# Performance work log

Hardware: AMD Instinct MI355X
Metric: run time of the kernel (lower is better)

Reference implementation:

```python
import jax, jax.numpy as jnp
import numpy as np

WS = 7            # window size (fixed by RelativeEmbedding default)
EMBED = 96
HEADS = 3
BATCH = 64
SIDE = 56         # height = width = sqrt(3136)
NEG_INF = float('-inf')


def _rel_bias_from_table(b_np):
    # Faithful reproduction of RelativeEmbedding.__init__ indexing quirks:
    # x = arange(1, ws+1, 1/ws) -> 49 floats; diffs truncated toward zero (.int())
    x = np.arange(1, WS + 1, 1.0 / WS, dtype=np.float32)
    xi = np.trunc(x[None, :] - x[:, None]).astype(np.int64)  # in [-6, 6]
    y = np.concatenate([np.arange(1, WS + 1)] * WS)
    yi = (y[None, :] - y[:, None]).astype(np.int64)          # in [-6, 6]
    n = 2 * WS - 1  # 13; emulate torch negative indexing with mod
    return b_np[xi % n, yi % n]  # (49, 49)


def _shift_masks():
    m = WS * (WS // 2)  # 21
    row_mask = np.zeros((WS * WS, WS * WS), dtype=np.float32)
    row_mask[-m:, :-m] = NEG_INF
    row_mask[:-m, -m:] = NEG_INF
    # rearrange '(r w1) (c w2) -> (w1 r) (w2 c)'
    col_mask = row_mask.reshape(WS, WS, WS, WS).transpose(1, 0, 3, 2).reshape(WS * WS, WS * WS)
    return jnp.asarray(row_mask), jnp.asarray(col_mask)


def setup_inputs() -> dict:
    key = jax.random.key(0)
    k1, k2, k3, k4, k5, k6 = jax.random.split(key, 6)
    x = jax.random.normal(k1, (BATCH, SIDE * SIDE, EMBED), dtype=jnp.float32)
    w1 = jax.random.normal(k2, (EMBED, 3 * EMBED), dtype=jnp.float32) * 0.02
    b1 = jnp.zeros((3 * EMBED,), dtype=jnp.float32)
    w2 = jax.random.normal(k3, (EMBED, EMBED), dtype=jnp.float32) * 0.02
    b2 = jnp.zeros((EMBED,), dtype=jnp.float32)
    b_table = np.asarray(jax.random.normal(k4, (2 * WS - 1, 2 * WS - 1), dtype=jnp.float32))
    rel_bias = jnp.asarray(_rel_bias_from_table(b_table))  # (49, 49), non-trainable
    return {"x": x, "w1": w1, "b1": b1, "w2": w2, "b2": b2, "rel_bias": rel_bias}


def reference(x, w1, b1, w2, b2, rel_bias):
    Bz, N, C = x.shape
    side = SIDE
    H = HEADS
    E = C // H          # head dim = 32
    nh = side // WS     # 8 windows per side

    qkv = x @ w1 + b1                                   # (B, N, 3C)
    # 'b (h w) (c K) -> b h w c K' with K=3 fastest-varying
    qkv = qkv.reshape(Bz, side, side, C, 3)
    # shifted-window roll; note (-7)//2 == -4 in Python (faithful to source)
    qkv = jnp.roll(qkv, ((-WS) // 2, (-WS) // 2), axis=(1, 2))
    # 'b (h m1) (w m2) (H E) K -> b H h w (m1 m2) E K'
    qkv = qkv.reshape(Bz, nh, WS, nh, WS, H, E, 3)
    qkv = qkv.transpose(0, 5, 1, 3, 2, 4, 6, 7).reshape(Bz, H, nh, nh, WS * WS, E, 3)
    q, k, v = qkv[..., 0], qkv[..., 1], qkv[..., 2]

    scale = jnp.sqrt(jnp.float32(E))
    att = jnp.einsum('bHhwme,bHhwne->bHhwmn', q, k) / scale  # (B,H,8,8,49,49)
    att = att + rel_bias

    row_mask, col_mask = _shift_masks()
    att = att.at[:, :, -1, :].add(row_mask)   # last window row
    att = att.at[:, :, :, -1].add(col_mask)   # last window column

    p = jax.nn.softmax(att, axis=-1)
    out = jnp.einsum('bHhwmn,bHhwne->bHhwme', p, v)          # (B,H,8,8,49,32)

    # 'b H h w (m1 m2) E -> b (h m1) (w m2) (H E)'
    out = out.reshape(Bz, H, nh, nh, WS, WS, E)
    out = out.transpose(0, 2, 4, 3, 5, 1, 6).reshape(Bz, side, side, C)
    # reverse roll uses +(7//2) == +3 (faithful asymmetry in the source)
    out = jnp.roll(out, (WS // 2, WS // 2), axis=(1, 2))
    out = out.reshape(Bz, N, C)
    return out @ w2 + b2
```

## Files before the change

### kernel.cpp

```cpp
#include <hip/hip_runtime.h>
#include <hip/hip_fp16.h>

typedef _Float16 half8_t __attribute__((ext_vector_type(8)));
typedef _Float16 half4_t __attribute__((ext_vector_type(4)));
typedef float f32x4 __attribute__((ext_vector_type(4)));
typedef unsigned int u32x4 __attribute__((ext_vector_type(4)));

#define WS_W2T 55296
#define WS_B1P 73728
#define WS_TBL 74880

__global__ __launch_bounds__(256) void swin_prep_kernel(
    const float* __restrict__ w1, const float* __restrict__ b1,
    const float* __restrict__ w2, const float* __restrict__ relb,
    _Float16* __restrict__ w1T, _Float16* __restrict__ w2T,
    float* __restrict__ b1p, float* __restrict__ tblP)
{
    int idx = blockIdx.x * 256 + threadIdx.x;
    const float L2E = 1.4426950408889634f;
    const float qs2 = 0.17677669529663687f * L2E;
    if (idx < 27648) {
        int jp = idx / 96, k = idx % 96;
        float v;
        if (jp < 96) {
            int f = jp >> 4, m = jp & 15;
            int cq = (f >> 1) * 32 + (m >> 2) * 8 + (f & 1) * 4 + (m & 3);
            v = w1[k * 288 + cq * 3] * qs2;
        } else {
            int jo = (jp % 96) * 3 + (jp / 96);
            v = w1[k * 288 + jo];
        }
        w1T[idx] = (_Float16)v;
    } else if (idx < 36864) {
        int i2 = idx - 27648;
        int n = i2 / 96, k = i2 % 96;
        w2T[i2] = (_Float16)w2[k * 96 + n];
    } else if (idx < 37152) {
        int jp = idx - 36864;
        float v = b1[(jp % 96) * 3 + (jp / 96)];
        if (jp < 96) v *= qs2;
        b1p[jp] = v;
    } else if (idx < 53536) {
        int t = idx - 37152;
        int vv = t >> 12, q = (t >> 6) & 63, c = t & 63;
        int i = c >> 4, m = c & 15;
        int k = (i >> 1) * 32 + (m >> 2) * 8 + (i & 1) * 4 + (m & 3);
        float val = -1e30f;
        if (q < 49 && k < 49) {
            val = relb[q * 49 + k] * L2E;
            if ((vv & 1) && ((q >= 28) != (k >= 28))) val = -1e30f;
            if ((vv & 2) && (((q % 7) >= 4) != ((k % 7) >= 4))) val = -1e30f;
        }
        tblP[t] = val;
    }
}

__device__ __forceinline__ unsigned int pack2h(float a, float b) {
    union { _Float16 h[2]; unsigned int u; } p;
    p.h[0] = (_Float16)a; p.h[1] = (_Float16)b;
    return p.u;
}
__device__ __forceinline__ unsigned int pkrtz(float a, float b) {
    return __builtin_bit_cast(unsigned int, __builtin_amdgcn_cvt_pkrtz(a, b));
}

__global__ __launch_bounds__(256) void swin_attn_kernel(
    const float* __restrict__ x,
    const _Float16* __restrict__ w1T,
    const _Float16* __restrict__ w2T,
    const float* __restrict__ b1p,
    const float* __restrict__ b2,
    const float* __restrict__ tblP,
    float* __restrict__ out)
{
    __shared__ __align__(16) char smem[27136];
    _Float16* Kb = (_Float16*)smem;
    _Float16* Vt = (_Float16*)(smem + 13312);
    _Float16* Xs = Kb;

    const int tid = threadIdx.x;
    const int wv = tid >> 6, lane = tid & 63;
    const int lr = lane & 15, lg = lane >> 4;

    const int gid = blockIdx.x;
    const int b = gid >> 6, wh = (gid >> 3) & 7, ww = gid & 7;
    const f32x4 fz = {0.f, 0.f, 0.f, 0.f};

    {
        const int p = tid >> 2, sub = tid & 3;
        const float* xrow = nullptr;
        if (p < 49) {
            const int m1 = p / 7, m2 = p % 7;
            int rr = wh * 7 + m1 + 4; if (rr >= 56) rr -= 56;
            int cc = ww * 7 + m2 + 4; if (cc >= 56) cc -= 56;
            xrow = x + ((size_t)b * 3136 + rr * 56 + cc) * 96;
        }
        #pragma unroll
        for (int j = 0; j < 6; ++j) {
            const int e = sub * 24 + j * 4;
            half4_t hv = {(_Float16)0.f, (_Float16)0.f, (_Float16)0.f, (_Float16)0.f};
            if (p < 49) {
                const float4 v = *(const float4*)(xrow + e);
                hv[0] = (_Float16)v.x; hv[1] = (_Float16)v.y;
                hv[2] = (_Float16)v.z; hv[3] = (_Float16)v.w;
            }
            *(half4_t*)(Xs + p * 104 + e) = hv;
        }
    }
    __syncthreads();

    half8_t xa[4][3], xq[3];
    #pragma unroll
    for (int mt = 0; mt < 4; ++mt)
        #pragma unroll
        for (int kt = 0; kt < 3; ++kt)
            xa[mt][kt] = *(const half8_t*)(Xs + (mt * 16 + lr) * 104 + kt * 32 + lg * 8);
    #pragma unroll
    for (int kt = 0; kt < 3; ++kt)
        xq[kt] = *(const half8_t*)(Xs + (wv * 16 + lr) * 104 + kt * 32 + lg * 8);
    __syncthreads();

    {
        half8_t bf0, bf1, bf2; float bv;
        {
            const int nt0 = 6 + wv;
            bf0 = *(const half8_t*)(w1T + (nt0 * 16 + lr) * 96 + lg * 8);
            bf1 = *(const half8_t*)(w1T + (nt0 * 16 + lr) * 96 + 32 + lg * 8);
            bf2 = *(const half8_t*)(w1T + (nt0 * 16 + lr) * 96 + 64 + lg * 8);
            bv = b1p[nt0 * 16 + lr];
        }
        #pragma unroll
        for (int t = 0; t < 3; ++t) {
            const int nt = 6 + wv + 4 * t;
            half8_t nf0 = bf0, nf1 = bf1, nf2 = bf2; float nbv = bv;
            if (t < 2) {
                const int ntn = nt + 4;
                nf0 = *(const half8_t*)(w1T + (ntn * 16 + lr) * 96 + lg * 8);
                nf1 = *(const half8_t*)(w1T + (ntn * 16 + lr) * 96 + 32 + lg * 8);
                nf2 = *(const half8_t*)(w1T + (ntn * 16 + lr) * 96 + 64 + lg * 8);
                nbv = b1p[ntn * 16 + lr];
            }
            #pragma unroll
            for (int mt = 0; mt < 4; ++mt) {
                f32x4 acc = fz;
                acc = __builtin_amdgcn_mfma_f32_16x16x32_f16(xa[mt][0], bf0, acc, 0, 0, 0);
                acc = __builtin_amdgcn_mfma_f32_16x16x32_f16(xa[mt][1], bf1, acc, 0, 0, 0);
                acc = __builtin_amdgcn_mfma_f32_16x16x32_f16(xa[mt][2], bf2, acc, 0, 0, 0);
                if (nt < 12) {
                    const int kc = ((nt - 6) * 16 + lr) ^ ((lg & 1) << 4);
                    #pragma unroll
                    for (int r = 0; r < 4; ++r) {
                        const int krow = ((mt >> 1) * 2 + (lg & 1)) * 16
                                       + ((mt * 2 + (lg >> 1)) & 3) * 4 + r;
                        Kb[krow * 104 + kc] = (_Float16)(acc[r] + bv);
                    }
                } else {
                    const int nv = nt - 12;
                    const int hh = nv >> 1, eta = nv & 1;
                    const int vrow = hh * 32 + ((lr >> 2) & 1) * 16
                                   + (((eta << 1) + (lr >> 3)) & 3) * 4 + (lr & 3);
                    half4_t hv;
                    #pragma unroll
                    for (int r = 0; r < 4; ++r) hv[r] = (_Float16)(acc[r] + bv);
                    *(half4_t*)(Vt + vrow * 72 + mt * 16 + lg * 4) = hv;
                }
            }
            bf0 = nf0; bf1 = nf1; bf2 = nf2; bv = nbv;
        }
    }

    unsigned int qpk[3][4];
    {
        half8_t af0 = *(const half8_t*)(w1T + lr * 96 + lg * 8);
        half8_t af1 = *(const half8_t*)(w1T + lr * 96 + 32 + lg * 8);
        half8_t af2 = *(const half8_t*)(w1T + lr * 96 + 64 + lg * 8);
        #pragma unroll
        for (int f = 0; f < 6; ++f) {
            half8_t n0 = af0, n1 = af1, n2 = af2;
            if (f < 5) {
                n0 = *(const half8_t*)(w1T + ((f + 1) * 16 + lr) * 96 + lg * 8);
                n1 = *(const half8_t*)(w1T + ((f + 1) * 16 + lr) * 96 + 32 + lg * 8);
                n2 = *(const half8_t*)(w1T + ((f + 1) * 16 + lr) * 96 + 64 + lg * 8);
            }
            f32x4 acc = fz;
            acc = __builtin_amdgcn_mfma_f32_16x16x32_f16(af0, xq[0], acc, 0, 0, 0);
            acc = __builtin_amdgcn_mfma_f32_16x16x32_f16(af1, xq[1], acc, 0, 0, 0);
            acc = __builtin_amdgcn_mfma_f32_16x16x32_f16(af2, xq[2], acc, 0, 0, 0);
            const float4 bq = *(const float4*)(b1p + (f >> 1) * 32 + lg * 8 + (f & 1) * 4);
            qpk[f >> 1][(f & 1) * 2 + 0] = pack2h(acc[0] + bq.x, acc[1] + bq.y);
            qpk[f >> 1][(f & 1) * 2 + 1] = pack2h(acc[2] + bq.z, acc[3] + bq.w);
            af0 = n0; af1 = n1; af2 = n2;
        }
    }

    f32x4 tv[4];
    {
        const float* tblv = tblP + ((wh == 7) ? 4096 : 0) + ((ww == 7) ? 8192 : 0)
                          + (wv * 16 + lr) * 64 + lg * 4;
        #pragma unroll
        for (int i = 0; i < 4; ++i)
            tv[i] = *(const f32x4*)(tblv + i * 16);
    }
    __syncthreads();

    f32x4 accO[6];
    #pragma unroll
    for (int i = 0; i < 6; ++i) accO[i] = fz;

    #pragma unroll
    for (int h = 0; h < 3; ++h) {
        const u32x4 qd = {qpk[h][0], qpk[h][1], qpk[h][2], qpk[h][3]};
        const half8_t qv = __builtin_bit_cast(half8_t, qd);

        f32x4 s[4];
        #pragma unroll
        for (int i = 0; i < 4; ++i) {
            const int col = (h * 32 + lg * 8) ^ ((i & 1) << 4);
            half8_t kf = *(const half8_t*)(Kb + (i * 16 + lr) * 104 + col);
            s[i] = __builtin_amdgcn_mfma_f32_16x16x32_f16(kf, qv, tv[i], 0, 0, 0);
        }
        half8_t vf00 = *(const half8_t*)(Vt + (h * 32 + lr) * 72 + lg * 8);
        half8_t vf01 = *(const half8_t*)(Vt + (h * 32 + lr) * 72 + 32 + lg * 8);
        half8_t vf10 = *(const half8_t*)(Vt + (h * 32 + 16 + lr) * 72 + lg * 8);
        half8_t vf11 = *(const half8_t*)(Vt + (h * 32 + 16 + lr) * 72 + 32 + lg * 8);
        half8_t wf[6];
        #pragma unroll
        for (int nt = 0; nt < 6; ++nt)
            wf[nt] = *(const half8_t*)(w2T + (nt * 16 + lr) * 96 + h * 32 + lg * 8);

        float ps[4];
        #pragma unroll
        for (int i = 0; i < 4; ++i) {
            float a0 = exp2f(s[i][0]), a1 = exp2f(s[i][1]);
            float a2 = exp2f(s[i][2]), a3 = exp2f(s[i][3]);
            s[i][0] = a0; s[i][1] = a1; s[i][2] = a2; s[i][3] = a3;
            ps[i] = (a0 + a1) + (a2 + a3);
        }
        float sum = (ps[0] + ps[1]) + (ps[2] + ps[3]);
        const u32x4 p0 = {pkrtz(s[0][0], s[0][1]), pkrtz(s[0][2], s[0][3]),
                          pkrtz(s[1][0], s[1][1]), pkrtz(s[1][2], s[1][3])};
        const u32x4 p1 = {pkrtz(s[2][0], s[2][1]), pkrtz(s[2][2], s[2][3]),
                          pkrtz(s[3][0], s[3][1]), pkrtz(s[3][2], s[3][3])};
        const half8_t pf0 = __builtin_bit_cast(half8_t, p0);
        const half8_t pf1 = __builtin_bit_cast(half8_t, p1);
        sum += __shfl_xor(sum, 16);
        sum += __shfl_xor(sum, 32);
        f32x4 o0 = __builtin_amdgcn_mfma_f32_16x16x32_f16(vf00, pf0, fz, 0, 0, 0);
        o0 = __builtin_amdgcn_mfma_f32_16x16x32_f16(vf01, pf1, o0, 0, 0, 0);
        f32x4 o1 = __builtin_amdgcn_mfma_f32_16x16x32_f16(vf10, pf0, fz, 0, 0, 0);
        o1 = __builtin_amdgcn_mfma_f32_16x16x32_f16(vf11, pf1, o1, 0, 0, 0);
        const float inv = 1.0f / sum;
        const u32x4 od = {pkrtz(o0[0] * inv, o0[1] * inv), pkrtz(o0[2] * inv, o0[3] * inv),
                          pkrtz(o1[0] * inv, o1[1] * inv), pkrtz(o1[2] * inv, o1[3] * inv)};
        const half8_t of = __builtin_bit_cast(half8_t, od);
        #pragma unroll
        for (int nt = 0; nt < 6; ++nt)
            accO[nt] = __builtin_amdgcn_mfma_f32_16x16x32_f16(of, wf[nt], accO[nt], 0, 0, 0);
    }

    float b2v[6];
    #pragma unroll
    for (int nt = 0; nt < 6; ++nt) b2v[nt] = b2[nt * 16 + lr];
    #pragma unroll
    for (int r = 0; r < 4; ++r) {
        const int row = wv * 16 + lg * 4 + r;
        if (row < 49) {
            const int m1 = row / 7, m2 = row % 7;
            int oi = wh * 7 + m1 + 3; if (oi >= 56) oi -= 56;
            int oj = ww * 7 + m2 + 3; if (oj >= 56) oj -= 56;
            float* op = out + ((size_t)b * 3136 + oi * 56 + oj) * 96;
            #pragma unroll
            for (int nt = 0; nt < 6; ++nt)
                op[nt * 16 + lr] = accO[nt][r] + b2v[nt];
        }
    }
}

extern "C" void kernel_launch(void* const* d_in, const int* in_sizes, int n_in,
                              void* d_out, int out_size, void* d_ws, size_t ws_size,
                              hipStream_t stream) {
    const float* x    = (const float*)d_in[0];
    const float* w1   = (const float*)d_in[1];
    const float* b1   = (const float*)d_in[2];
    const float* w2   = (const float*)d_in[3];
    const float* b2   = (const float*)d_in[4];
    const float* relb = (const float*)d_in[5];
    float* out = (float*)d_out;

    _Float16* w1T  = (_Float16*)((char*)d_ws);
    _Float16* w2T  = (_Float16*)((char*)d_ws + WS_W2T);
    float*    b1p  = (float*)((char*)d_ws + WS_B1P);
    float*    tblP = (float*)((char*)d_ws + WS_TBL);

    swin_prep_kernel<<<210, 256, 0, stream>>>(w1, b1, w2, relb, w1T, w2T, b1p, tblP);
    swin_attn_kernel<<<4096, 256, 0, stream>>>(x, w1T, w2T, b1p, b2, tblP, out);
}
```

Baseline: 83.29 us.

## Split fused window attention into separate QKV and attention kernels via workspace

Divides the single fused kernel into a QKV projection kernel that writes per-window K/V shared-memory images and Q fragments to global workspace, and an attention kernel that reloads them. The aim is to shorten each kernel's register and instruction footprint so each stage can schedule and occupy the GPU better. In exchange it adds large global write and read traffic for the intermediate tensors plus a second launch. The original fused kernel is kept as a fallback when the workspace is too small.

```diff
diff --git a/kernel.cpp b/kernel.cpp
--- a/kernel.cpp
+++ b/kernel.cpp
@@ -9,6 +9,10 @@
 #define WS_W2T 55296
 #define WS_B1P 73728
 #define WS_TBL 74880
+#define WS_KVG 140416
+#define KV_BYTES 27136
+#define WS_QG  111289472ULL
+#define WS_NEED 161621120ULL
 
 __global__ __launch_bounds__(256) void swin_prep_kernel(
     const float* __restrict__ w1, const float* __restrict__ b1,
@@ -64,14 +68,11 @@
     return __builtin_bit_cast(unsigned int, __builtin_amdgcn_cvt_pkrtz(a, b));
 }
 
-__global__ __launch_bounds__(256) void swin_attn_kernel(
+__global__ __launch_bounds__(256) void swin_qkv_kernel(
     const float* __restrict__ x,
     const _Float16* __restrict__ w1T,
-    const _Float16* __restrict__ w2T,
     const float* __restrict__ b1p,
-    const float* __restrict__ b2,
-    const float* __restrict__ tblP,
-    float* __restrict__ out)
+    char* __restrict__ kvg, unsigned int* __restrict__ qg)
 {
     __shared__ __align__(16) char smem[27136];
     _Float16* Kb = (_Float16*)smem;
@@ -81,7 +82,6 @@
     const int tid = threadIdx.x;
     const int wv = tid >> 6, lane = tid & 63;
     const int lr = lane & 15, lg = lane >> 4;
-
     const int gid = blockIdx.x;
     const int b = gid >> 6, wh = (gid >> 3) & 7, ww = gid & 7;
     const f32x4 fz = {0.f, 0.f, 0.f, 0.f};
@@ -192,7 +192,55 @@
             af0 = n0; af1 = n1; af2 = n2;
         }
     }
-
+    {
+        unsigned int* qdst = qg + (size_t)gid * 3072 + tid * 12;
+        *(u32x4*)(qdst + 0) = (u32x4){qpk[0][0], qpk[0][1], qpk[0][2], qpk[0][3]};
+        *(u32x4*)(qdst + 4) = (u32x4){qpk[1][0], qpk[1][1], qpk[1][2], qpk[1][3]};
+        *(u32x4*)(qdst + 8) = (u32x4){qpk[2][0], qpk[2][1], qpk[2][2], qpk[2][3]};
+    }
+    __syncthreads();
+
+    {
+        char* dst = kvg + (size_t)gid * KV_BYTES;
+        #pragma unroll
+        for (int i = 0; i < 7; ++i) {
+            const int idx = tid + i * 256;
+            if (idx < 1696)
+                *(float4*)(dst + idx * 16) = *(const float4*)(smem + idx * 16);
+        }
+    }
+}
+
+__global__ __launch_bounds__(256) void swin_attn2_kernel(
+    const char* __restrict__ kvg, const unsigned int* __restrict__ qg,
+    const _Float16* __restrict__ w2T, const float* __restrict__ b2,
+    const float* __restrict__ tblP, float* __restrict__ out)
+{
+    __shared__ __align__(16) char smem[27136];
+    _Float16* Kb = (_Float16*)smem;
+    _Float16* Vt = (_Float16*)(smem + 13312);
+
+    const int tid = threadIdx.x;
+    const int wv = tid >> 6, lane = tid & 63;
+    const int lr = lane & 15, lg = lane >> 4;
+    const int gid = blockIdx.x;
+    const int b = gid >> 6, wh = (gid >> 3) & 7, ww = gid & 7;
+    const f32x4 fz = {0.f, 0.f, 0.f, 0.f};
+
+    float4 stg[7];
+    const char* src = kvg + (size_t)gid * KV_BYTES;
+    #pragma unroll
+    for (int i = 0; i < 7; ++i) {
+        const int idx = tid + i * 256;
+        if (idx < 1696) stg[i] = *(const float4*)(src + idx * 16);
+    }
+    u32x4 qd[3];
+    {
+        const unsigned int* qsrc = qg + (size_t)gid * 3072 + tid * 12;
+        qd[0] = *(const u32x4*)(qsrc + 0);
+        qd[1] = *(const u32x4*)(qsrc + 4);
+        qd[2] = *(const u32x4*)(qsrc + 8);
+    }
     f32x4 tv[4];
     {
         const float* tblv = tblP + ((wh == 7) ? 4096 : 0) + ((ww == 7) ? 8192 : 0)
@@ -201,6 +249,11 @@
         for (int i = 0; i < 4; ++i)
             tv[i] = *(const f32x4*)(tblv + i * 16);
     }
+    #pragma unroll
+    for (int i = 0; i < 7; ++i) {
+        const int idx = tid + i * 256;
+        if (idx < 1696) *(float4*)(smem + idx * 16) = stg[i];
+    }
     __syncthreads();
 
     f32x4 accO[6];
@@ -209,9 +262,7 @@
 
     #pragma unroll
     for (int h = 0; h < 3; ++h) {
-        const u32x4 qd = {qpk[h][0], qpk[h][1], qpk[h][2], qpk[h][3]};
-        const half8_t qv = __builtin_bit_cast(half8_t, qd);
-
+        const half8_t qv = __builtin_bit_cast(half8_t, qd[h]);
         f32x4 s[4];
         #pragma unroll
         for (int i = 0; i < 4; ++i) {
@@ -276,6 +327,208 @@
     }
 }
 
+__global__ __launch_bounds__(256) void swin_attn_kernel(
+    const float* __restrict__ x,
+    const _Float16* __restrict__ w1T,
+    const _Float16* __restrict__ w2T,
+    const float* __restrict__ b1p,
+    const float* __restrict__ b2,
+    const float* __restrict__ tblP,
+    float* __restrict__ out)
+{
+    __shared__ __align__(16) char smem[27136];
+    _Float16* Kb = (_Float16*)smem;
+    _Float16* Vt = (_Float16*)(smem + 13312);
+    _Float16* Xs = Kb;
+
+    const int tid = threadIdx.x;
+    const int wv = tid >> 6, lane = tid & 63;
+    const int lr = lane & 15, lg = lane >> 4;
+    const int gid = blockIdx.x;
+    const int b = gid >> 6, wh = (gid >> 3) & 7, ww = gid & 7;
+    const f32x4 fz = {0.f, 0.f, 0.f, 0.f};
+
+    {
+        const int p = tid >> 2, sub = tid & 3;
+        const float* xrow = nullptr;
+        if (p < 49) {
+            const int m1 = p / 7, m2 = p % 7;
+            int rr = wh * 7 + m1 + 4; if (rr >= 56) rr -= 56;
+            int cc = ww * 7 + m2 + 4; if (cc >= 56) cc -= 56;
+            xrow = x + ((size_t)b * 3136 + rr * 56 + cc) * 96;
+        }
+        #pragma unroll
+        for (int j = 0; j < 6; ++j) {
+            const int e = sub * 24 + j * 4;
+            half4_t hv = {(_Float16)0.f, (_Float16)0.f, (_Float16)0.f, (_Float16)0.f};
+            if (p < 49) {
+                const float4 v = *(const float4*)(xrow + e);
+                hv[0] = (_Float16)v.x; hv[1] = (_Float16)v.y;
+                hv[2] = (_Float16)v.z; hv[3] = (_Float16)v.w;
+            }
+            *(half4_t*)(Xs + p * 104 + e) = hv;
+        }
+    }
+    __syncthreads();
+    half8_t xa[4][3], xq[3];
+    #pragma unroll
+    for (int mt = 0; mt < 4; ++mt)
+        #pragma unroll
+        for (int kt = 0; kt < 3; ++kt)
+            xa[mt][kt] = *(const half8_t*)(Xs + (mt * 16 + lr) * 104 + kt * 32 + lg * 8);
+    #pragma unroll
+    for (int kt = 0; kt < 3; ++kt)
+        xq[kt] = *(const half8_t*)(Xs + (wv * 16 + lr) * 104 + kt * 32 + lg * 8);
+    __syncthreads();
+    {
+        half8_t bf0, bf1, bf2; float bv;
+        {
+            const int nt0 = 6 + wv;
+            bf0 = *(const half8_t*)(w1T + (nt0 * 16 + lr) * 96 + lg * 8);
+            bf1 = *(const half8_t*)(w1T + (nt0 * 16 + lr) * 96 + 32 + lg * 8);
+            bf2 = *(const half8_t*)(w1T + (nt0 * 16 + lr) * 96 + 64 + lg * 8);
+            bv = b1p[nt0 * 16 + lr];
+        }
+        #pragma unroll
+        for (int t = 0; t < 3; ++t) {
+            const int nt = 6 + wv + 4 * t;
+            half8_t nf0 = bf0, nf1 = bf1, nf2 = bf2; float nbv = bv;
+            if (t < 2) {
+                const int ntn = nt + 4;
+                nf0 = *(const half8_t*)(w1T + (ntn * 16 + lr) * 96 + lg * 8);
+                nf1 = *(const half8_t*)(w1T + (ntn * 16 + lr) * 96 + 32 + lg * 8);
+                nf2 = *(const half8_t*)(w1T + (ntn * 16 + lr) * 96 + 64 + lg * 8);
+                nbv = b1p[ntn * 16 + lr];
+            }
+            #pragma unroll
+            for (int mt = 0; mt < 4; ++mt) {
+                f32x4 acc = fz;
+                acc = __builtin_amdgcn_mfma_f32_16x16x32_f16(xa[mt][0], bf0, acc, 0, 0, 0);
+                acc = __builtin_amdgcn_mfma_f32_16x16x32_f16(xa[mt][1], bf1, acc, 0, 0, 0);
+                acc = __builtin_amdgcn_mfma_f32_16x16x32_f16(xa[mt][2], bf2, acc, 0, 0, 0);
+                if (nt < 12) {
+                    const int kc = ((nt - 6) * 16 + lr) ^ ((lg & 1) << 4);
+                    #pragma unroll
+                    for (int r = 0; r < 4; ++r) {
+                        const int krow = ((mt >> 1) * 2 + (lg & 1)) * 16
+                                       + ((mt * 2 + (lg >> 1)) & 3) * 4 + r;
+                        Kb[krow * 104 + kc] = (_Float16)(acc[r] + bv);
+                    }
+                } else {
+                    const int nv = nt - 12;
+                    const int hh = nv >> 1, eta = nv & 1;
+                    const int vrow = hh * 32 + ((lr >> 2) & 1) * 16
+                                   + (((eta << 1) + (lr >> 3)) & 3) * 4 + (lr & 3);
+                    half4_t hv;
+                    #pragma unroll
+                    for (int r = 0; r < 4; ++r) hv[r] = (_Float16)(acc[r] + bv);
+                    *(half4_t*)(Vt + vrow * 72 + mt * 16 + lg * 4) = hv;
+                }
+            }
+            bf0 = nf0; bf1 = nf1; bf2 = nf2; bv = nbv;
+        }
+    }
+    unsigned int qpk[3][4];
+    {
+        half8_t af0 = *(const half8_t*)(w1T + lr * 96 + lg * 8);
+        half8_t af1 = *(const half8_t*)(w1T + lr * 96 + 32 + lg * 8);
+        half8_t af2 = *(const half8_t*)(w1T + lr * 96 + 64 + lg * 8);
+        #pragma unroll
+        for (int f = 0; f < 6; ++f) {
+            half8_t n0 = af0, n1 = af1, n2 = af2;
+            if (f < 5) {
+                n0 = *(const half8_t*)(w1T + ((f + 1) * 16 + lr) * 96 + lg * 8);
+                n1 = *(const half8_t*)(w1T + ((f + 1) * 16 + lr) * 96 + 32 + lg * 8);
+                n2 = *(const half8_t*)(w1T + ((f + 1) * 16 + lr) * 96 + 64 + lg * 8);
+            }
+            f32x4 acc = fz;
+            acc = __builtin_amdgcn_mfma_f32_16x16x32_f16(af0, xq[0], acc, 0, 0, 0);
+            acc = __builtin_amdgcn_mfma_f32_16x16x32_f16(af1, xq[1], acc, 0, 0, 0);
+            acc = __builtin_amdgcn_mfma_f32_16x16x32_f16(af2, xq[2], acc, 0, 0, 0);
+            const float4 bq = *(const float4*)(b1p + (f >> 1) * 32 + lg * 8 + (f & 1) * 4);
+            qpk[f >> 1][(f & 1) * 2 + 0] = pack2h(acc[0] + bq.x, acc[1] + bq.y);
+            qpk[f >> 1][(f & 1) * 2 + 1] = pack2h(acc[2] + bq.z, acc[3] + bq.w);
+            af0 = n0; af1 = n1; af2 = n2;
+        }
+    }
+    f32x4 tv[4];
+    {
+        const float* tblv = tblP + ((wh == 7) ? 4096 : 0) + ((ww == 7) ? 8192 : 0)
+                          + (wv * 16 + lr) * 64 + lg * 4;
+        #pragma unroll
+        for (int i = 0; i < 4; ++i)
+            tv[i] = *(const f32x4*)(tblv + i * 16);
+    }
+    __syncthreads();
+    f32x4 accO[6];
+    #pragma unroll
+    for (int i = 0; i < 6; ++i) accO[i] = fz;
+    #pragma unroll
+    for (int h = 0; h < 3; ++h) {
+        const u32x4 qdv = {qpk[h][0], qpk[h][1], qpk[h][2], qpk[h][3]};
+        const half8_t qv = __builtin_bit_cast(half8_t, qdv);
+        f32x4 s[4];
+        #pragma unroll
+        for (int i = 0; i < 4; ++i) {
+            const int col = (h * 32 + lg * 8) ^ ((i & 1) << 4);
+            half8_t kf = *(const half8_t*)(Kb + (i * 16 + lr) * 104 + col);
+            s[i] = __builtin_amdgcn_mfma_f32_16x16x32_f16(kf, qv, tv[i], 0, 0, 0);
+        }
+        half8_t vf00 = *(const half8_t*)(Vt + (h * 32 + lr) * 72 + lg * 8);
+        half8_t vf01 = *(const half8_t*)(Vt + (h * 32 + lr) * 72 + 32 + lg * 8);
+        half8_t vf10 = *(const half8_t*)(Vt + (h * 32 + 16 + lr) * 72 + lg * 8);
+        half8_t vf11 = *(const half8_t*)(Vt + (h * 32 + 16 + lr) * 72 + 32 + lg * 8);
+        half8_t wf[6];
+        #pragma unroll
+        for (int nt = 0; nt < 6; ++nt)
+            wf[nt] = *(const half8_t*)(w2T + (nt * 16 + lr) * 96 + h * 32 + lg * 8);
+        float ps[4];
+        #pragma unroll
+        for (int i = 0; i < 4; ++i) {
+            float a0 = exp2f(s[i][0]), a1 = exp2f(s[i][1]);
+            float a2 = exp2f(s[i][2]), a3 = exp2f(s[i][3]);
+            s[i][0] = a0; s[i][1] = a1; s[i][2] = a2; s[i][3] = a3;
+            ps[i] = (a0 + a1) + (a2 + a3);
+        }
+        float sum = (ps[0] + ps[1]) + (ps[2] + ps[3]);
+        const u32x4 p0 = {pkrtz(s[0][0], s[0][1]), pkrtz(s[0][2], s[0][3]),
+                          pkrtz(s[1][0], s[1][1]), pkrtz(s[1][2], s[1][3])};
+        const u32x4 p1 = {pkrtz(s[2][0], s[2][1]), pkrtz(s[2][2], s[2][3]),
+                          pkrtz(s[3][0], s[3][1]), pkrtz(s[3][2], s[3][3])};
+        const half8_t pf0 = __builtin_bit_cast(half8_t, p0);
+        const half8_t pf1 = __builtin_bit_cast(half8_t, p1);
+        sum += __shfl_xor(sum, 16);
+        sum += __shfl_xor(sum, 32);
+        f32x4 o0 = __builtin_amdgcn_mfma_f32_16x16x32_f16(vf00, pf0, fz, 0, 0, 0);
+        o0 = __builtin_amdgcn_mfma_f32_16x16x32_f16(vf01, pf1, o0, 0, 0, 0);
+        f32x4 o1 = __builtin_amdgcn_mfma_f32_16x16x32_f16(vf10, pf0, fz, 0, 0, 0);
+        o1 = __builtin_amdgcn_mfma_f32_16x16x32_f16(vf11, pf1, o1, 0, 0, 0);
+        const float inv = 1.0f / sum;
+        const u32x4 od = {pkrtz(o0[0] * inv, o0[1] * inv), pkrtz(o0[2] * inv, o0[3] * inv),
+                          pkrtz(o1[0] * inv, o1[1] * inv), pkrtz(o1[2] * inv, o1[3] * inv)};
+        const half8_t of = __builtin_bit_cast(half8_t, od);
+        #pragma unroll
+        for (int nt = 0; nt < 6; ++nt)
+            accO[nt] = __builtin_amdgcn_mfma_f32_16x16x32_f16(of, wf[nt], accO[nt], 0, 0, 0);
+    }
+    float b2v[6];
+    #pragma unroll
+    for (int nt = 0; nt < 6; ++nt) b2v[nt] = b2[nt * 16 + lr];
+    #pragma unroll
+    for (int r = 0; r < 4; ++r) {
+        const int row = wv * 16 + lg * 4 + r;
+        if (row < 49) {
+            const int m1 = row / 7, m2 = row % 7;
+            int oi = wh * 7 + m1 + 3; if (oi >= 56) oi -= 56;
+            int oj = ww * 7 + m2 + 3; if (oj >= 56) oj -= 56;
+            float* op = out + ((size_t)b * 3136 + oi * 56 + oj) * 96;
+            #pragma unroll
+            for (int nt = 0; nt < 6; ++nt)
+                op[nt * 16 + lr] = accO[nt][r] + b2v[nt];
+        }
+    }
+}
+
 extern "C" void kernel_launch(void* const* d_in, const int* in_sizes, int n_in,
                               void* d_out, int out_size, void* d_ws, size_t ws_size,
                               hipStream_t stream) {
@@ -293,5 +546,13 @@
     float*    tblP = (float*)((char*)d_ws + WS_TBL);
 
     swin_prep_kernel<<<210, 256, 0, stream>>>(w1, b1, w2, relb, w1T, w2T, b1p, tblP);
-    swin_attn_kernel<<<4096, 256, 0, stream>>>(x, w1T, w2T, b1p, b2, tblP, out);
-}
+
+    if (ws_size >= WS_NEED) {
+        char*         kvg = (char*)d_ws + WS_KVG;
+        unsigned int* qg  = (unsigned int*)((char*)d_ws + WS_QG);
+        swin_qkv_kernel<<<4096, 256, 0, stream>>>(x, w1T, b1p, kvg, qg);
+        swin_attn2_kernel<<<4096, 256, 0, stream>>>(kvg, qg, w2T, b2, tblP, out);
+    } else {
+        swin_attn_kernel<<<4096, 256, 0, stream>>>(x, w1T, w2T, b1p, b2, tblP, out);
+    }
+}
```

Result: slower. 165.2 us (+98.3%).

## Process four windows per block and prefetch next window's input during attention

Applied to the files above, without the earlier changes.

Each block now handles four consecutive windows along the row instead of one, giving Xs its own shared buffer separate from K and V. The next window's x tile is loaded and converted into shared memory while the current window's attention and output projection run, aiming to hide global load latency. This also amortises per-block setup such as the b2 loads. The trade-offs are a quarter as many blocks (1024), a larger LDS footprint that may reduce occupancy, and dropping the weight-fragment register prefetch.

```diff
diff --git a/kernel.cpp b/kernel.cpp
--- a/kernel.cpp
+++ b/kernel.cpp
@@ -73,73 +73,71 @@
     const float* __restrict__ tblP,
     float* __restrict__ out)
 {
-    __shared__ __align__(16) char smem[27136];
-    _Float16* Kb = (_Float16*)smem;
-    _Float16* Vt = (_Float16*)(smem + 13312);
-    _Float16* Xs = Kb;
+    __shared__ __align__(16) char smem[40448];
+    _Float16* Xs = (_Float16*)smem;
+    _Float16* Kb = (_Float16*)(smem + 13312);
+    _Float16* Vt = (_Float16*)(smem + 26624);
 
     const int tid = threadIdx.x;
     const int wv = tid >> 6, lane = tid & 63;
     const int lr = lane & 15, lg = lane >> 4;
 
-    const int gid = blockIdx.x;
-    const int b = gid >> 6, wh = (gid >> 3) & 7, ww = gid & 7;
+    const int gid0 = blockIdx.x * 4;
+    const int b = gid0 >> 6, wh = (gid0 >> 3) & 7, ww0 = gid0 & 7;
     const f32x4 fz = {0.f, 0.f, 0.f, 0.f};
 
+    const int sp = tid >> 2, ssub = tid & 3;
+    int srr = 0, sm2 = 0;
+    if (sp < 49) {
+        const int m1 = sp / 7; sm2 = sp % 7;
+        srr = wh * 7 + m1 + 4; if (srr >= 56) srr -= 56;
+    }
+
     {
-        const int p = tid >> 2, sub = tid & 3;
         const float* xrow = nullptr;
-        if (p < 49) {
-            const int m1 = p / 7, m2 = p % 7;
-            int rr = wh * 7 + m1 + 4; if (rr >= 56) rr -= 56;
-            int cc = ww * 7 + m2 + 4; if (cc >= 56) cc -= 56;
-            xrow = x + ((size_t)b * 3136 + rr * 56 + cc) * 96;
+        if (sp < 49) {
+            int cc = ww0 * 7 + sm2 + 4; if (cc >= 56) cc -= 56;
+            xrow = x + ((size_t)b * 3136 + srr * 56 + cc) * 96;
         }
         #pragma unroll
         for (int j = 0; j < 6; ++j) {
-            const int e = sub * 24 + j * 4;
+            const int e = ssub * 24 + j * 4;
             half4_t hv = {(_Float16)0.f, (_Float16)0.f, (_Float16)0.f, (_Float16)0.f};
-            if (p < 49) {
+            if (sp < 49) {
                 const float4 v = *(const float4*)(xrow + e);
                 hv[0] = (_Float16)v.x; hv[1] = (_Float16)v.y;
                 hv[2] = (_Float16)v.z; hv[3] = (_Float16)v.w;
             }
-            *(half4_t*)(Xs + p * 104 + e) = hv;
+            *(half4_t*)(Xs + sp * 104 + e) = hv;
         }
     }
     __syncthreads();
 
-    half8_t xa[4][3], xq[3];
+    float b2v[6];
     #pragma unroll
-    for (int mt = 0; mt < 4; ++mt)
+    for (int nt = 0; nt < 6; ++nt) b2v[nt] = b2[nt * 16 + lr];
+
+    #pragma unroll 1
+    for (int n = 0; n < 4; ++n) {
+        const int ww = ww0 + n;
+
+        half8_t xa[4][3], xq[3];
+        #pragma unroll
+        for (int mt = 0; mt < 4; ++mt)
+            #pragma unroll
+            for (int kt = 0; kt < 3; ++kt)
+                xa[mt][kt] = *(const half8_t*)(Xs + (mt * 16 + lr) * 104 + kt * 32 + lg * 8);
         #pragma unroll
         for (int kt = 0; kt < 3; ++kt)
-            xa[mt][kt] = *(const half8_t*)(Xs + (mt * 16 + lr) * 104 + kt * 32 + lg * 8);
-    #pragma unroll
-    for (int kt = 0; kt < 3; ++kt)
-        xq[kt] = *(const half8_t*)(Xs + (wv * 16 + lr) * 104 + kt * 32 + lg * 8);
-    __syncthreads();
-
-    {
-        half8_t bf0, bf1, bf2; float bv;
-        {
-            const int nt0 = 6 + wv;
-            bf0 = *(const half8_t*)(w1T + (nt0 * 16 + lr) * 96 + lg * 8);
-            bf1 = *(const half8_t*)(w1T + (nt0 * 16 + lr) * 96 + 32 + lg * 8);
-            bf2 = *(const half8_t*)(w1T + (nt0 * 16 + lr) * 96 + 64 + lg * 8);
-            bv = b1p[nt0 * 16 + lr];
-        }
+            xq[kt] = *(const half8_t*)(Xs + (wv * 16 + lr) * 104 + kt * 32 + lg * 8);
+
         #pragma unroll
         for (int t = 0; t < 3; ++t) {
             const int nt = 6 + wv + 4 * t;
-            half8_t nf0 = bf0, nf1 = bf1, nf2 = bf2; float nbv = bv;
-            if (t < 2) {
-                const int ntn = nt + 4;
-                nf0 = *(const half8_t*)(w1T + (ntn * 16 + lr) * 96 + lg * 8);
-                nf1 = *(const half8_t*)(w1T + (ntn * 16 + lr) * 96 + 32 + lg * 8);
-                nf2 = *(const half8_t*)(w1T + (ntn * 16 + lr) * 96 + 64 + lg * 8);
-                nbv = b1p[ntn * 16 + lr];
-            }
+            half8_t bf0 = *(const half8_t*)(w1T + (nt * 16 + lr) * 96 + lg * 8);
+            half8_t bf1 = *(const half8_t*)(w1T + (nt * 16 + lr) * 96 + 32 + lg * 8);
+            half8_t bf2 = *(const half8_t*)(w1T + (nt * 16 + lr) * 96 + 64 + lg * 8);
+            const float bv = b1p[nt * 16 + lr];
             #pragma unroll
             for (int mt = 0; mt < 4; ++mt) {
                 f32x4 acc = fz;
@@ -165,23 +163,14 @@
                     *(half4_t*)(Vt + vrow * 72 + mt * 16 + lg * 4) = hv;
                 }
             }
-            bf0 = nf0; bf1 = nf1; bf2 = nf2; bv = nbv;
-        }
-    }
-
-    unsigned int qpk[3][4];
-    {
-        half8_t af0 = *(const half8_t*)(w1T + lr * 96 + lg * 8);
-        half8_t af1 = *(const half8_t*)(w1T + lr * 96 + 32 + lg * 8);
-        half8_t af2 = *(const half8_t*)(w1T + lr * 96 + 64 + lg * 8);
+        }
+
+        unsigned int qpk[3][4];
         #pragma unroll
         for (int f = 0; f < 6; ++f) {
-            half8_t n0 = af0, n1 = af1, n2 = af2;
-            if (f < 5) {
-                n0 = *(const half8_t*)(w1T + ((f + 1) * 16 + lr) * 96 + lg * 8);
-                n1 = *(const half8_t*)(w1T + ((f + 1) * 16 + lr) * 96 + 32 + lg * 8);
-                n2 = *(const half8_t*)(w1T + ((f + 1) * 16 + lr) * 96 + 64 + lg * 8);
-            }
+            half8_t af0 = *(const half8_t*)(w1T + (f * 16 + lr) * 96 + lg * 8);
+            half8_t af1 = *(const half8_t*)(w1T + (f * 16 + lr) * 96 + 32 + lg * 8);
+            half8_t af2 = *(const half8_t*)(w1T + (f * 16 + lr) * 96 + 64 + lg * 8);
             f32x4 acc = fz;
             acc = __builtin_amdgcn_mfma_f32_16x16x32_f16(af0, xq[0], acc, 0, 0, 0);
             acc = __builtin_amdgcn_mfma_f32_16x16x32_f16(af1, xq[1], acc, 0, 0, 0);
@@ -189,90 +178,105 @@
             const float4 bq = *(const float4*)(b1p + (f >> 1) * 32 + lg * 8 + (f & 1) * 4);
             qpk[f >> 1][(f & 1) * 2 + 0] = pack2h(acc[0] + bq.x, acc[1] + bq.y);
             qpk[f >> 1][(f & 1) * 2 + 1] = pack2h(acc[2] + bq.z, acc[3] + bq.w);
-            af0 = n0; af1 = n1; af2 = n2;
-        }
-    }
-
-    f32x4 tv[4];
-    {
-        const float* tblv = tblP + ((wh == 7) ? 4096 : 0) + ((ww == 7) ? 8192 : 0)
-                          + (wv * 16 + lr) * 64 + lg * 4;
-        #pragma unroll
-        for (int i = 0; i < 4; ++i)
-            tv[i] = *(const f32x4*)(tblv + i * 16);
-    }
-    __syncthreads();
-
-    f32x4 accO[6];
-    #pragma unroll
-    for (int i = 0; i < 6; ++i) accO[i] = fz;
-
-    #pragma unroll
-    for (int h = 0; h < 3; ++h) {
-        const u32x4 qd = {qpk[h][0], qpk[h][1], qpk[h][2], qpk[h][3]};
-        const half8_t qv = __builtin_bit_cast(half8_t, qd);
-
-        f32x4 s[4];
-        #pragma unroll
-        for (int i = 0; i < 4; ++i) {
-            const int col = (h * 32 + lg * 8) ^ ((i & 1) << 4);
-            half8_t kf = *(const half8_t*)(Kb + (i * 16 + lr) * 104 + col);
-            s[i] = __builtin_amdgcn_mfma_f32_16x16x32_f16(kf, qv, tv[i], 0, 0, 0);
-        }
-        half8_t vf00 = *(const half8_t*)(Vt + (h * 32 + lr) * 72 + lg * 8);
-        half8_t vf01 = *(const half8_t*)(Vt + (h * 32 + lr) * 72 + 32 + lg * 8);
-        half8_t vf10 = *(const half8_t*)(Vt + (h * 32 + 16 + lr) * 72 + lg * 8);
-        half8_t vf11 = *(const half8_t*)(Vt + (h * 32 + 16 + lr) * 72 + 32 + lg * 8);
-        half8_t wf[6];
-        #pragma unroll
-        for (int nt = 0; nt < 6; ++nt)
-            wf[nt] = *(const half8_t*)(w2T + (nt * 16 + lr) * 96 + h * 32 + lg * 8);
-
-        float ps[4];
-        #pragma unroll
-        for (int i = 0; i < 4; ++i) {
-            float a0 = exp2f(s[i][0]), a1 = exp2f(s[i][1]);
-            float a2 = exp2f(s[i][2]), a3 = exp2f(s[i][3]);
-            s[i][0] = a0; s[i][1] = a1; s[i][2] = a2; s[i][3] = a3;
-            ps[i] = (a0 + a1) + (a2 + a3);
-        }
-        float sum = (ps[0] + ps[1]) + (ps[2] + ps[3]);
-        const u32x4 p0 = {pkrtz(s[0][0], s[0][1]), pkrtz(s[0][2], s[0][3]),
-                          pkrtz(s[1][0], s[1][1]), pkrtz(s[1][2], s[1][3])};
-        const u32x4 p1 = {pkrtz(s[2][0], s[2][1]), pkrtz(s[2][2], s[2][3]),
-                          pkrtz(s[3][0], s[3][1]), pkrtz(s[3][2], s[3][3])};
-        const half8_t pf0 = __builtin_bit_cast(half8_t, p0);
-        const half8_t pf1 = __builtin_bit_cast(half8_t, p1);
-        sum += __shfl_xor(sum, 16);
-        sum += __shfl_xor(sum, 32);
-        f32x4 o0 = __builtin_amdgcn_mfma_f32_16x16x32_f16(vf00, pf0, fz, 0, 0, 0);
-        o0 = __builtin_amdgcn_mfma_f32_16x16x32_f16(vf01, pf1, o0, 0, 0, 0);
-        f32x4 o1 = __builtin_amdgcn_mfma_f32_16x16x32_f16(vf10, pf0, fz, 0, 0, 0);
-        o1 = __builtin_amdgcn_mfma_f32_16x16x32_f16(vf11, pf1, o1, 0, 0, 0);
-        const float inv = 1.0f / sum;
-        const u32x4 od = {pkrtz(o0[0] * inv, o0[1] * inv), pkrtz(o0[2] * inv, o0[3] * inv),
-                          pkrtz(o1[0] * inv, o1[1] * inv), pkrtz(o1[2] * inv, o1[3] * inv)};
-        const half8_t of = __builtin_bit_cast(half8_t, od);
-        #pragma unroll
-        for (int nt = 0; nt < 6; ++nt)
-            accO[nt] = __builtin_amdgcn_mfma_f32_16x16x32_f16(of, wf[nt], accO[nt], 0, 0, 0);
-    }
-
-    float b2v[6];
-    #pragma unroll
-    for (int nt = 0; nt < 6; ++nt) b2v[nt] = b2[nt * 16 + lr];
-    #pragma unroll
-    for (int r = 0; r < 4; ++r) {
-        const int row = wv * 16 + lg * 4 + r;
-        if (row < 49) {
-            const int m1 = row / 7, m2 = row % 7;
-            int oi = wh * 7 + m1 + 3; if (oi >= 56) oi -= 56;
-            int oj = ww * 7 + m2 + 3; if (oj >= 56) oj -= 56;
-            float* op = out + ((size_t)b * 3136 + oi * 56 + oj) * 96;
+        }
+
+        f32x4 tv[4];
+        {
+            const float* tblv = tblP + ((wh == 7) ? 4096 : 0) + ((ww == 7) ? 8192 : 0)
+                              + (wv * 16 + lr) * 64 + lg * 4;
+            #pragma unroll
+            for (int i = 0; i < 4; ++i)
+                tv[i] = *(const f32x4*)(tblv + i * 16);
+        }
+        __syncthreads();
+
+        if (n < 3) {
+            const float* xrow = nullptr;
+            if (sp < 49) {
+                int cc = (ww + 1) * 7 + sm2 + 4; if (cc >= 56) cc -= 56;
+                xrow = x + ((size_t)b * 3136 + srr * 56 + cc) * 96;
+            }
+            #pragma unroll
+            for (int j = 0; j < 6; ++j) {
+                const int e = ssub * 24 + j * 4;
+                half4_t hv = {(_Float16)0.f, (_Float16)0.f, (_Float16)0.f, (_Float16)0.f};
+                if (sp < 49) {
+                    const float4 v = *(const float4*)(xrow + e);
+                    hv[0] = (_Float16)v.x; hv[1] = (_Float16)v.y;
+                    hv[2] = (_Float16)v.z; hv[3] = (_Float16)v.w;
+                }
+                *(half4_t*)(Xs + sp * 104 + e) = hv;
+            }
+        }
+
+        f32x4 accO[6];
+        #pragma unroll
+        for (int i = 0; i < 6; ++i) accO[i] = fz;
+
+        #pragma unroll
+        for (int h = 0; h < 3; ++h) {
+            const u32x4 qd = {qpk[h][0], qpk[h][1], qpk[h][2], qpk[h][3]};
+            const half8_t qv = __builtin_bit_cast(half8_t, qd);
+            f32x4 s[4];
+            #pragma unroll
+            for (int i = 0; i < 4; ++i) {
+                const int col = (h * 32 + lg * 8) ^ ((i & 1) << 4);
+                half8_t kf = *(const half8_t*)(Kb + (i * 16 + lr) * 104 + col);
+                s[i] = __builtin_amdgcn_mfma_f32_16x16x32_f16(kf, qv, tv[i], 0, 0, 0);
+            }
+            half8_t vf00 = *(const half8_t*)(Vt + (h * 32 + lr) * 72 + lg * 8);
+            half8_t vf01 = *(const half8_t*)(Vt + (h * 32 + lr) * 72 + 32 + lg * 8);
+            half8_t vf10 = *(const half8_t*)(Vt + (h * 32 + 16 + lr) * 72 + lg * 8);
+            half8_t vf11 = *(const half8_t*)(Vt + (h * 32 + 16 + lr) * 72 + 32 + lg * 8);
+            half8_t wf[6];
             #pragma unroll
             for (int nt = 0; nt < 6; ++nt)
-                op[nt * 16 + lr] = accO[nt][r] + b2v[nt];
-        }
+                wf[nt] = *(const half8_t*)(w2T + (nt * 16 + lr) * 96 + h * 32 + lg * 8);
+
+            float ps[4];
+            #pragma unroll
+            for (int i = 0; i < 4; ++i) {
+                float a0 = exp2f(s[i][0]), a1 = exp2f(s[i][1]);
+                float a2 = exp2f(s[i][2]), a3 = exp2f(s[i][3]);
+                s[i][0] = a0; s[i][1] = a1; s[i][2] = a2; s[i][3] = a3;
+                ps[i] = (a0 + a1) + (a2 + a3);
+            }
+            float sum = (ps[0] + ps[1]) + (ps[2] + ps[3]);
+            const u32x4 p0 = {pkrtz(s[0][0], s[0][1]), pkrtz(s[0][2], s[0][3]),
+                              pkrtz(s[1][0], s[1][1]), pkrtz(s[1][2], s[1][3])};
+            const u32x4 p1 = {pkrtz(s[2][0], s[2][1]), pkrtz(s[2][2], s[2][3]),
+                              pkrtz(s[3][0], s[3][1]), pkrtz(s[3][2], s[3][3])};
+            const half8_t pf0 = __builtin_bit_cast(half8_t, p0);
+            const half8_t pf1 = __builtin_bit_cast(half8_t, p1);
+            sum += __shfl_xor(sum, 16);
+            sum += __shfl_xor(sum, 32);
+            f32x4 o0 = __builtin_amdgcn_mfma_f32_16x16x32_f16(vf00, pf0, fz, 0, 0, 0);
+            o0 = __builtin_amdgcn_mfma_f32_16x16x32_f16(vf01, pf1, o0, 0, 0, 0);
+            f32x4 o1 = __builtin_amdgcn_mfma_f32_16x16x32_f16(vf10, pf0, fz, 0, 0, 0);
+            o1 = __builtin_amdgcn_mfma_f32_16x16x32_f16(vf11, pf1, o1, 0, 0, 0);
+            const float inv = 1.0f / sum;
+            const u32x4 od = {pkrtz(o0[0] * inv, o0[1] * inv), pkrtz(o0[2] * inv, o0[3] * inv),
+                              pkrtz(o1[0] * inv, o1[1] * inv), pkrtz(o1[2] * inv, o1[3] * inv)};
+            const half8_t of = __builtin_bit_cast(half8_t, od);
+            #pragma unroll
+            for (int nt = 0; nt < 6; ++nt)
+                accO[nt] = __builtin_amdgcn_mfma_f32_16x16x32_f16(of, wf[nt], accO[nt], 0, 0, 0);
+        }
+
+        #pragma unroll
+        for (int r = 0; r < 4; ++r) {
+            const int row = wv * 16 + lg * 4 + r;
+            if (row < 49) {
+                const int m1 = row / 7, m2 = row % 7;
+                int oi = wh * 7 + m1 + 3; if (oi >= 56) oi -= 56;
+                int oj = ww * 7 + m2 + 3; if (oj >= 56) oj -= 56;
+                float* op = out + ((size_t)b * 3136 + oi * 56 + oj) * 96;
+                #pragma unroll
+                for (int nt = 0; nt < 6; ++nt)
+                    op[nt * 16 + lr] = accO[nt][r] + b2v[nt];
+            }
+        }
+        __syncthreads();
     }
 }
 
@@ -293,5 +297,5 @@
     float*    tblP = (float*)((char*)d_ws + WS_TBL);
 
     swin_prep_kernel<<<210, 256, 0, stream>>>(w1, b1, w2, relb, w1T, w2T, b1p, tblP);
-    swin_attn_kernel<<<4096, 256, 0, stream>>>(x, w1T, w2T, b1p, b2, tblP, out);
-}
+    swin_attn_kernel<<<1024, 256, 0, stream>>>(x, w1T, w2T, b1p, b2, tblP, out);
+}
```

Measured after the change: 93.49 us. 12.2% more time.
